# Kernel optimization log

Hardware: AMD Instinct MI355X
Metric: run time of the kernel (lower is better)

Reference implementation:

```python
import jax, jax.numpy as jnp
import numpy as np

EPS = 1e-5

def _conv1x1(x, w, b=None):
    # x: (B, Cin, H, W), w: (Cout, Cin) -> (B, Cout, H, W)
    y = jnp.einsum('bchw,oc->bohw', x, w)
    if b is not None:
        y = y + b[None, :, None, None]
    return y

def setup_inputs() -> dict:
    key = jax.random.key(0)
    ks = jax.random.split(key, 14)
    B, C, I = 4, 256, 128
    Ha = Wa = 64
    Hd = Wd = 128
    s = 0.05
    return {
        'detect':  jax.random.normal(ks[0], (B, C, Hd, Wd), jnp.float32),
        'aim':     jax.random.normal(ks[1], (B, C, Ha, Wa), jnp.float32),
        'g_w':     jax.random.normal(ks[2], (I, C), jnp.float32) * s,
        'g_b':     jax.random.normal(ks[3], (I,), jnp.float32) * s,
        'theta_w': jax.random.normal(ks[4], (I, C), jnp.float32) * s,
        'theta_b': jax.random.normal(ks[5], (I,), jnp.float32) * s,
        'phi_w':   jax.random.normal(ks[6], (I, C), jnp.float32) * s,
        'phi_b':   jax.random.normal(ks[7], (I,), jnp.float32) * s,
        'q_w':     jax.random.normal(ks[8], (C, I), jnp.float32) * s,
        'q_b':     jax.random.normal(ks[9], (C,), jnp.float32) * s,
        'bn_gamma': jax.random.normal(ks[10], (C,), jnp.float32),
        'bn_beta':  jax.random.normal(ks[11], (C,), jnp.float32),
        'bn_mean':  jax.random.normal(ks[12], (C,), jnp.float32),
        'bn_var':   jax.random.uniform(ks[13], (C,), jnp.float32) + 0.5,
    }

def reference(detect, aim, g_w, g_b, theta_w, theta_b, phi_w, phi_b,
              q_w, q_b, bn_gamma, bn_beta, bn_mean, bn_var):
    B, C, Hd, Wd = detect.shape
    _, _, Ha, Wa = aim.shape
    Na = Ha * Wa
    Nd = Hd * Wd
    I = g_w.shape[0]

    # 1x1 conv projections, flattened to token sequences
    a_g   = _conv1x1(aim, g_w, g_b).reshape(B, I, Na)        # g(aim)
    th_a  = _conv1x1(aim, theta_w, theta_b).reshape(B, I, Na)
    ph_d  = _conv1x1(detect, phi_w, phi_b).reshape(B, I, Nd)
    # (d_x = g(detect) is dead code in the original forward; omitted)

    # f = theta_x @ phi_x : (B, Na, Nd); permuted -> (B, Nd, Na); N = Na
    f = jnp.einsum('bia,bid->bad', th_a, ph_d)               # (B, Na, Nd)
    inv_n = jnp.float32(1.0 / Na)
    # non_det = (f^T / Na) @ a_x : (B, Nd, I) -> permute -> (B, I, Nd)
    non = jnp.einsum('bad,bia->bid', f * inv_n, a_g)         # (B, I, Nd)
    non = non.reshape(B, I, Hd, Wd)

    # Q: 1x1 conv (I -> C) + BatchNorm (inference mode, running stats)
    y = _conv1x1(non, q_w, q_b)
    inv_std = jax.lax.rsqrt(bn_var + EPS)
    y = (y - bn_mean[None, :, None, None]) * (bn_gamma * inv_std)[None, :, None, None] \
        + bn_beta[None, :, None, None]

    return y + detect
```

## Files before the change

### kernel.cpp

```cpp
#include <hip/hip_runtime.h>

constexpr int BB   = 4;
constexpr int CCH  = 256;
constexpr int IDIM = 128;
constexpr int NAa  = 4096;
constexpr int NDd  = 16384;
constexpr int PAD  = 320;
constexpr float NAinv = 1.0f / 4096.0f;

typedef __bf16 bf16x8 __attribute__((ext_vector_type(8)));
typedef float  f32x4  __attribute__((ext_vector_type(4)));

__device__ inline unsigned short f2bfu(float f) {
    unsigned u = __float_as_uint(f);
    u += 0x7FFFu + ((u >> 16) & 1u);
    return (unsigned short)(u >> 16);
}

__global__ __launch_bounds__(256) void k_conv(const float* __restrict__ aim,
                                              unsigned short* __restrict__ Abf,
                                              float* __restrict__ r) {
    const int row = blockIdx.x;
    const float* src = aim + (long)row * NAa;
    unsigned short* dst = Abf + (long)row * NAa;
    const int t = threadIdx.x;
    float s = 0.f;
    #pragma unroll
    for (int j = 0; j < 4; ++j) {
        const int e = (j * 256 + t) * 4;
        float4 v = *(const float4*)(src + e);
        s += v.x + v.y + v.z + v.w;
        ushort4 o; o.x = f2bfu(v.x); o.y = f2bfu(v.y); o.z = f2bfu(v.z); o.w = f2bfu(v.w);
        *(ushort4*)(dst + e) = o;
    }
    __shared__ float red[256];
    red[t] = s; __syncthreads();
    for (int st = 128; st > 0; st >>= 1) { if (t < st) red[t] += red[t + st]; __syncthreads(); }
    if (t == 0) r[row] = red[0];
}

__global__ __launch_bounds__(256) void k_prep(const float* __restrict__ qw,
                                              const float* __restrict__ gw,
                                              const float* __restrict__ gb,
                                              const float* __restrict__ thw,
                                              const float* __restrict__ thb,
                                              const float* __restrict__ phw,
                                              const float* __restrict__ phb,
                                              unsigned short* __restrict__ Ph,
                                              unsigned short* __restrict__ Rt) {
    const int idx = blockIdx.x * 256 + threadIdx.x;
    if (idx < CCH * PAD) {
        const int o = idx / PAD, c = idx - o * PAD;
        float acc = 0.f;
        if (c <= 256) {
            for (int i = 0; i < IDIM; ++i)
                acc += qw[o * IDIM + i] * ((c < 256) ? gw[i * CCH + c] : gb[i]);
        }
        Ph[idx] = f2bfu(acc);
    } else {
        const int id2 = idx - CCH * PAD;
        const int c2 = id2 / PAD, k = id2 - c2 * PAD;
        float acc = 0.f;
        if (k <= 256 && c2 <= 256) {
            for (int i = 0; i < IDIM; ++i) {
                const float av = (k < 256) ? thw[i * CCH + k] : thb[i];
                const float bv = (c2 < 256) ? phw[i * CCH + c2] : phb[i];
                acc += av * bv;
            }
        }
        Rt[id2] = f2bfu(acc);
    }
}

__global__ __launch_bounds__(64) void k_S(const unsigned short* __restrict__ Abf,
                                          float* __restrict__ Spart) {
    const int z = blockIdx.z, b = z >> 3, chunk = z & 7;
    const unsigned short* A = Abf + (long)b * CCH * NAa;
    const int lane = threadIdx.x, quad = lane >> 4, l16 = lane & 15;
    const int mb = blockIdx.y * 64, nb = blockIdx.x * 64;
    const int kb = chunk * 512;
    f32x4 acc[4][4] = {};
    for (int ks = 0; ks < 16; ++ks) {
        const int k = kb + ks * 32 + quad * 8;
        bf16x8 af[4], bfr[4];
        #pragma unroll
        for (int i = 0; i < 4; ++i) af[i]  = *(const bf16x8*)(A + (long)(mb + i * 16 + l16) * NAa + k);
        #pragma unroll
        for (int j = 0; j < 4; ++j) bfr[j] = *(const bf16x8*)(A + (long)(nb + j * 16 + l16) * NAa + k);
        #pragma unroll
        for (int i = 0; i < 4; ++i)
            #pragma unroll
            for (int j = 0; j < 4; ++j)
                acc[i][j] = __builtin_amdgcn_mfma_f32_16x16x32_bf16(af[i], bfr[j], acc[i][j], 0, 0, 0);
    }
    float* o = Spart + (long)z * CCH * CCH;
    #pragma unroll
    for (int i = 0; i < 4; ++i)
        #pragma unroll
        for (int j = 0; j < 4; ++j)
            #pragma unroll
            for (int reg = 0; reg < 4; ++reg)
                o[(long)(mb + i * 16 + quad * 4 + reg) * CCH + nb + j * 16 + l16] = acc[i][j][reg];
}

__global__ __launch_bounds__(256) void k_red(const float* __restrict__ Spart,
                                             const float* __restrict__ r,
                                             unsigned short* __restrict__ Shat) {
    const int b = blockIdx.y;
    const int idx = blockIdx.x * 256 + threadIdx.x;
    const int k = idx / PAD, n = idx - k * PAD;
    float v = 0.f;
    if (k < 256 && n < 256) {
        #pragma unroll
        for (int p = 0; p < 8; ++p)
            v += Spart[(long)(b * 8 + p) * CCH * CCH + k * CCH + n];
    } else if (k == 256 && n < 256) v = r[b * CCH + n];
    else if (n == 256 && k < 256)   v = r[b * CCH + k];
    else if (k == 256 && n == 256)  v = 4096.0f;
    Shat[(long)b * PAD * PAD + idx] = f2bfu(v);
}

__global__ __launch_bounds__(64) void k_t1(const unsigned short* __restrict__ Ph,
                                           const unsigned short* __restrict__ Sh,
                                           unsigned short* __restrict__ Th) {
    const int b = blockIdx.z;
    const unsigned short* S = Sh + (long)b * PAD * PAD;
    unsigned short* T = Th + (long)b * CCH * PAD;
    const int n0 = blockIdx.x * 64, m0 = blockIdx.y * 64;
    const int lane = threadIdx.x, quad = lane >> 4, l16 = lane & 15;
    f32x4 acc[4][4] = {};
    for (int kt = 0; kt < PAD; kt += 32) {
        bf16x8 af[4], bfr[4];
        #pragma unroll
        for (int i = 0; i < 4; ++i) af[i]  = *(const bf16x8*)(Ph + (long)(m0 + i * 16 + l16) * PAD + kt + quad * 8);
        #pragma unroll
        for (int j = 0; j < 4; ++j) bfr[j] = *(const bf16x8*)(S  + (long)(n0 + j * 16 + l16) * PAD + kt + quad * 8);
        #pragma unroll
        for (int i = 0; i < 4; ++i)
            #pragma unroll
            for (int j = 0; j < 4; ++j)
                acc[i][j] = __builtin_amdgcn_mfma_f32_16x16x32_bf16(af[i], bfr[j], acc[i][j], 0, 0, 0);
    }
    #pragma unroll
    for (int i = 0; i < 4; ++i)
        #pragma unroll
        for (int j = 0; j < 4; ++j)
            #pragma unroll
            for (int reg = 0; reg < 4; ++reg)
                T[(long)(m0 + i * 16 + quad * 4 + reg) * PAD + n0 + j * 16 + l16] = f2bfu(acc[i][j][reg]);
}

__global__ __launch_bounds__(64) void k_t2(const unsigned short* __restrict__ Th,
                                           const unsigned short* __restrict__ Rt,
                                           const float* __restrict__ qb,
                                           const float* __restrict__ gamma,
                                           const float* __restrict__ beta,
                                           const float* __restrict__ mean,
                                           const float* __restrict__ var,
                                           unsigned short* __restrict__ W5u,
                                           float* __restrict__ b5) {
    const int b = blockIdx.z;
    const unsigned short* A = Th + (long)b * CCH * PAD;
    const int n0 = blockIdx.x * 64, m0 = blockIdx.y * 64;
    const int lane = threadIdx.x, quad = lane >> 4, l16 = lane & 15;
    f32x4 acc[4][4] = {};
    for (int kt = 0; kt < PAD; kt += 32) {
        bf16x8 af[4], bfr[4];
        #pragma unroll
        for (int i = 0; i < 4; ++i) af[i]  = *(const bf16x8*)(A  + (long)(m0 + i * 16 + l16) * PAD + kt + quad * 8);
        #pragma unroll
        for (int j = 0; j < 4; ++j) bfr[j] = *(const bf16x8*)(Rt + (long)(n0 + j * 16 + l16) * PAD + kt + quad * 8);
        #pragma unroll
        for (int i = 0; i < 4; ++i)
            #pragma unroll
            for (int j = 0; j < 4; ++j)
                acc[i][j] = __builtin_amdgcn_mfma_f32_16x16x32_bf16(af[i], bfr[j], acc[i][j], 0, 0, 0);
    }
    #pragma unroll
    for (int i = 0; i < 4; ++i) {
        #pragma unroll
        for (int reg = 0; reg < 4; ++reg) {
            const int o = m0 + i * 16 + quad * 4 + reg;
            const float s = gamma[o] * rsqrtf(var[o] + 1e-5f);
            #pragma unroll
            for (int j = 0; j < 4; ++j) {
                const int c2 = n0 + j * 16 + l16;
                const float val = acc[i][j][reg] * s * NAinv;
                if (c2 < CCH)
                    W5u[((long)b * CCH + o) * CCH + c2] = f2bfu(val + (o == c2 ? 1.0f : 0.0f));
                else if (c2 == CCH)
                    b5[b * CCH + o] = val + s * (qb[o] - mean[o]) + beta[o];
            }
        }
    }
}

__global__ __launch_bounds__(256) void k_final(const float* __restrict__ D0,
                                               const unsigned short* __restrict__ W5u,
                                               const float* __restrict__ b5,
                                               float* __restrict__ out) {
    const int z = blockIdx.z;
    const int nb = blockIdx.x * 128;
    const int ob = blockIdx.y * 128;
    const float* D = D0 + (long)z * CCH * NDd;
    float* O = out + (long)z * CCH * NDd;
    const unsigned short* W = W5u + (long)z * CCH * CCH;
    const int t = threadIdx.x, wv = t >> 6, lane = t & 63, quad = lane >> 4, l16 = lane & 15;
    const int mw = (wv >> 1) * 64, nw = (wv & 1) * 64;
    const int r2 = t >> 4, g = t & 15;
    __shared__ __align__(16) unsigned short lb[2][128][40];
    f32x4 x[4];

    auto load_tile = [&](int kt) {
        const float* base = D + (long)(kt + 2 * r2) * NDd + nb + 8 * g;
        x[0] = *(const f32x4*)(base);
        x[1] = *(const f32x4*)(base + NDd);
        x[2] = *(const f32x4*)(base + 4);
        x[3] = *(const f32x4*)(base + NDd + 4);
    };
    auto write_tile = [&](int buf) {
        #pragma unroll
        for (int e2 = 0; e2 < 2; ++e2)
            #pragma unroll
            for (int c = 0; c < 4; ++c) {
                const int n = 8 * g + 4 * e2 + c;
                const int p = ((n & 7) << 4) + (n >> 3);
                const unsigned v = (unsigned)f2bfu(x[2 * e2][c]) |
                                   ((unsigned)f2bfu(x[2 * e2 + 1][c]) << 16);
                *(unsigned*)&lb[buf][p][2 * r2] = v;
            }
    };

    int pj[4];
    #pragma unroll
    for (int j = 0; j < 4; ++j) {
        const int n = nw + j * 16 + l16;
        pj[j] = ((n & 7) << 4) + (n >> 3);
    }

    f32x4 acc[4][4] = {};
    load_tile(0);
    write_tile(0);
    load_tile(32);
    for (int it = 0; it < 8; ++it) {
        __syncthreads();
        const int kt = it * 32;
        bf16x8 af[4], bfr[4];
        #pragma unroll
        for (int i = 0; i < 4; ++i)
            af[i] = *(const bf16x8*)(W + (long)(ob + mw + i * 16 + l16) * CCH + kt + quad * 8);
        #pragma unroll
        for (int j = 0; j < 4; ++j)
            bfr[j] = *(const bf16x8*)&lb[it & 1][pj[j]][quad * 8];
        #pragma unroll
        for (int i = 0; i < 4; ++i)
            #pragma unroll
            for (int j = 0; j < 4; ++j)
                acc[i][j] = __builtin_amdgcn_mfma_f32_16x16x32_bf16(af[i], bfr[j], acc[i][j], 0, 0, 0);
        if (it < 7) {
            write_tile((it + 1) & 1);
            if (it < 6) load_tile((it + 2) * 32);
        }
    }
    #pragma unroll
    for (int i = 0; i < 4; ++i) {
        float bv[4];
        #pragma unroll
        for (int reg = 0; reg < 4; ++reg)
            bv[reg] = b5[z * CCH + ob + mw + i * 16 + quad * 4 + reg];
        #pragma unroll
        for (int j = 0; j < 4; ++j) {
            const int n = nb + nw + j * 16 + l16;
            #pragma unroll
            for (int reg = 0; reg < 4; ++reg)
                O[(long)(ob + mw + i * 16 + quad * 4 + reg) * NDd + n] = acc[i][j][reg] + bv[reg];
        }
    }
}

extern "C" void kernel_launch(void* const* d_in, const int* in_sizes, int n_in,
                              void* d_out, int out_size, void* d_ws, size_t ws_size,
                              hipStream_t stream) {
    const float* detect = (const float*)d_in[0];
    const float* aim    = (const float*)d_in[1];
    const float* g_w    = (const float*)d_in[2];
    const float* g_b    = (const float*)d_in[3];
    const float* th_w   = (const float*)d_in[4];
    const float* th_b   = (const float*)d_in[5];
    const float* phi_w  = (const float*)d_in[6];
    const float* phi_b  = (const float*)d_in[7];
    const float* q_w    = (const float*)d_in[8];
    const float* q_b    = (const float*)d_in[9];
    const float* gamma  = (const float*)d_in[10];
    const float* beta   = (const float*)d_in[11];
    const float* mean   = (const float*)d_in[12];
    const float* var    = (const float*)d_in[13];
    float* out = (float*)d_out;

    float* ws = (float*)d_ws;
    unsigned short* Abf = (unsigned short*)ws;
    float* r     = ws + 2097152;
    float* Spart = r + 1024;
    unsigned short* ub = (unsigned short*)(Spart + 2097152);
    unsigned short* Shat_u  = ub;
    unsigned short* Phat_u  = Shat_u + 409600;
    unsigned short* RhatT_u = Phat_u + 81920;
    unsigned short* That_u  = RhatT_u + 102400;
    unsigned short* W5u     = That_u + 327680;
    float* b5 = (float*)(W5u + 262144);

    k_prep<<<dim3((CCH * PAD + PAD * PAD) / 256), dim3(256), 0, stream>>>(
        q_w, g_w, g_b, th_w, th_b, phi_w, phi_b, Phat_u, RhatT_u);
    k_conv<<<dim3(BB * CCH), dim3(256), 0, stream>>>(aim, Abf, r);
    k_S<<<dim3(4, 4, BB * 8), dim3(64), 0, stream>>>(Abf, Spart);
    k_red<<<dim3(PAD * PAD / 256, BB), dim3(256), 0, stream>>>(Spart, r, Shat_u);
    k_t1<<<dim3(5, 4, BB), dim3(64), 0, stream>>>(Phat_u, Shat_u, That_u);
    k_t2<<<dim3(5, 4, BB), dim3(64), 0, stream>>>(That_u, RhatT_u, q_b, gamma, beta, mean, var, W5u, b5);
    k_final<<<dim3(NDd / 128, CCH / 128, BB), dim3(256), 0, stream>>>(detect, W5u, b5, out);
}
```

Measured before the change: 218.3 us.

## Merge front kernels, fuse T1/T2 via LDS, split S finer, simplify final load

Merges the aim conversion and weight-prep kernels into one launch, and fuses the two small 320-wide GEMMs (k_t1/k_t2) into a single kernel that keeps the intermediate T tile in shared memory instead of global. It also doubles the K-split of the Gram-matrix kernel to 16 chunks for more parallelism, at the cost of a larger partial-sum buffer and reduction. The final kernel drops its double-buffered LDS staging of detect and instead loads strided fp32 values directly into registers and packs them to bf16. The direct loads are column-strided per lane and may lose coalescing compared with the previous staged path.

```diff
diff --git a/kernel.cpp b/kernel.cpp
--- a/kernel.cpp
+++ b/kernel.cpp
@@ -17,70 +17,71 @@
     return (unsigned short)(u >> 16);
 }
 
-__global__ __launch_bounds__(256) void k_conv(const float* __restrict__ aim,
-                                              unsigned short* __restrict__ Abf,
-                                              float* __restrict__ r) {
-    const int row = blockIdx.x;
-    const float* src = aim + (long)row * NAa;
-    unsigned short* dst = Abf + (long)row * NAa;
+__global__ __launch_bounds__(256) void k_front(const float* __restrict__ aim,
+                                               unsigned short* __restrict__ Abf,
+                                               float* __restrict__ r,
+                                               const float* __restrict__ qw,
+                                               const float* __restrict__ gw,
+                                               const float* __restrict__ gb,
+                                               const float* __restrict__ thw,
+                                               const float* __restrict__ thb,
+                                               const float* __restrict__ phw,
+                                               const float* __restrict__ phb,
+                                               unsigned short* __restrict__ Ph,
+                                               unsigned short* __restrict__ Rt) {
     const int t = threadIdx.x;
-    float s = 0.f;
-    #pragma unroll
-    for (int j = 0; j < 4; ++j) {
-        const int e = (j * 256 + t) * 4;
-        float4 v = *(const float4*)(src + e);
-        s += v.x + v.y + v.z + v.w;
-        ushort4 o; o.x = f2bfu(v.x); o.y = f2bfu(v.y); o.z = f2bfu(v.z); o.w = f2bfu(v.w);
-        *(ushort4*)(dst + e) = o;
-    }
-    __shared__ float red[256];
-    red[t] = s; __syncthreads();
-    for (int st = 128; st > 0; st >>= 1) { if (t < st) red[t] += red[t + st]; __syncthreads(); }
-    if (t == 0) r[row] = red[0];
-}
-
-__global__ __launch_bounds__(256) void k_prep(const float* __restrict__ qw,
-                                              const float* __restrict__ gw,
-                                              const float* __restrict__ gb,
-                                              const float* __restrict__ thw,
-                                              const float* __restrict__ thb,
-                                              const float* __restrict__ phw,
-                                              const float* __restrict__ phb,
-                                              unsigned short* __restrict__ Ph,
-                                              unsigned short* __restrict__ Rt) {
-    const int idx = blockIdx.x * 256 + threadIdx.x;
-    if (idx < CCH * PAD) {
-        const int o = idx / PAD, c = idx - o * PAD;
-        float acc = 0.f;
-        if (c <= 256) {
-            for (int i = 0; i < IDIM; ++i)
-                acc += qw[o * IDIM + i] * ((c < 256) ? gw[i * CCH + c] : gb[i]);
-        }
-        Ph[idx] = f2bfu(acc);
+    if (blockIdx.x < BB * CCH) {
+        const int row = blockIdx.x;
+        const float* src = aim + (long)row * NAa;
+        unsigned short* dst = Abf + (long)row * NAa;
+        float s = 0.f;
+        #pragma unroll
+        for (int j = 0; j < 4; ++j) {
+            const int e = (j * 256 + t) * 4;
+            float4 v = *(const float4*)(src + e);
+            s += v.x + v.y + v.z + v.w;
+            ushort4 o; o.x = f2bfu(v.x); o.y = f2bfu(v.y); o.z = f2bfu(v.z); o.w = f2bfu(v.w);
+            *(ushort4*)(dst + e) = o;
+        }
+        __shared__ float red[256];
+        red[t] = s; __syncthreads();
+        for (int st = 128; st > 0; st >>= 1) { if (t < st) red[t] += red[t + st]; __syncthreads(); }
+        if (t == 0) r[row] = red[0];
     } else {
-        const int id2 = idx - CCH * PAD;
-        const int c2 = id2 / PAD, k = id2 - c2 * PAD;
-        float acc = 0.f;
-        if (k <= 256 && c2 <= 256) {
-            for (int i = 0; i < IDIM; ++i) {
-                const float av = (k < 256) ? thw[i * CCH + k] : thb[i];
-                const float bv = (c2 < 256) ? phw[i * CCH + c2] : phb[i];
-                acc += av * bv;
+        const int idx = (blockIdx.x - BB * CCH) * 256 + t;
+        if (idx < CCH * PAD) {
+            const int o = idx / PAD, c = idx - o * PAD;
+            float acc = 0.f;
+            if (c <= 256) {
+                for (int i = 0; i < IDIM; ++i)
+                    acc += qw[o * IDIM + i] * ((c < 256) ? gw[i * CCH + c] : gb[i]);
             }
-        }
-        Rt[id2] = f2bfu(acc);
+            Ph[idx] = f2bfu(acc);
+        } else {
+            const int id2 = idx - CCH * PAD;
+            const int c2 = id2 / PAD, k = id2 - c2 * PAD;
+            float acc = 0.f;
+            if (k <= 256 && c2 <= 256) {
+                for (int i = 0; i < IDIM; ++i) {
+                    const float av = (k < 256) ? thw[i * CCH + k] : thb[i];
+                    const float bv = (c2 < 256) ? phw[i * CCH + c2] : phb[i];
+                    acc += av * bv;
+                }
+            }
+            Rt[id2] = f2bfu(acc);
+        }
     }
 }
 
 __global__ __launch_bounds__(64) void k_S(const unsigned short* __restrict__ Abf,
                                           float* __restrict__ Spart) {
-    const int z = blockIdx.z, b = z >> 3, chunk = z & 7;
+    const int z = blockIdx.z, b = z >> 4, chunk = z & 15;
     const unsigned short* A = Abf + (long)b * CCH * NAa;
     const int lane = threadIdx.x, quad = lane >> 4, l16 = lane & 15;
     const int mb = blockIdx.y * 64, nb = blockIdx.x * 64;
-    const int kb = chunk * 512;
+    const int kb = chunk * 256;
     f32x4 acc[4][4] = {};
-    for (int ks = 0; ks < 16; ++ks) {
+    for (int ks = 0; ks < 8; ++ks) {
         const int k = kb + ks * 32 + quad * 8;
         bf16x8 af[4], bfr[4];
         #pragma unroll
@@ -112,86 +113,86 @@
     float v = 0.f;
     if (k < 256 && n < 256) {
         #pragma unroll
-        for (int p = 0; p < 8; ++p)
-            v += Spart[(long)(b * 8 + p) * CCH * CCH + k * CCH + n];
+        for (int p = 0; p < 16; ++p)
+            v += Spart[(long)(b * 16 + p) * CCH * CCH + k * CCH + n];
     } else if (k == 256 && n < 256) v = r[b * CCH + n];
     else if (n == 256 && k < 256)   v = r[b * CCH + k];
     else if (k == 256 && n == 256)  v = 4096.0f;
     Shat[(long)b * PAD * PAD + idx] = f2bfu(v);
 }
 
-__global__ __launch_bounds__(64) void k_t1(const unsigned short* __restrict__ Ph,
-                                           const unsigned short* __restrict__ Sh,
-                                           unsigned short* __restrict__ Th) {
-    const int b = blockIdx.z;
+__global__ __launch_bounds__(256) void k_w5f(const unsigned short* __restrict__ Ph,
+                                             const unsigned short* __restrict__ Sh,
+                                             const unsigned short* __restrict__ Rt,
+                                             const float* __restrict__ qb,
+                                             const float* __restrict__ gamma,
+                                             const float* __restrict__ beta,
+                                             const float* __restrict__ mean,
+                                             const float* __restrict__ var,
+                                             unsigned short* __restrict__ W5u,
+                                             float* __restrict__ b5) {
+    const int b = blockIdx.y, m0 = blockIdx.x * 64;
     const unsigned short* S = Sh + (long)b * PAD * PAD;
-    unsigned short* T = Th + (long)b * CCH * PAD;
-    const int n0 = blockIdx.x * 64, m0 = blockIdx.y * 64;
-    const int lane = threadIdx.x, quad = lane >> 4, l16 = lane & 15;
-    f32x4 acc[4][4] = {};
-    for (int kt = 0; kt < PAD; kt += 32) {
-        bf16x8 af[4], bfr[4];
-        #pragma unroll
-        for (int i = 0; i < 4; ++i) af[i]  = *(const bf16x8*)(Ph + (long)(m0 + i * 16 + l16) * PAD + kt + quad * 8);
-        #pragma unroll
-        for (int j = 0; j < 4; ++j) bfr[j] = *(const bf16x8*)(S  + (long)(n0 + j * 16 + l16) * PAD + kt + quad * 8);
-        #pragma unroll
-        for (int i = 0; i < 4; ++i)
-            #pragma unroll
-            for (int j = 0; j < 4; ++j)
-                acc[i][j] = __builtin_amdgcn_mfma_f32_16x16x32_bf16(af[i], bfr[j], acc[i][j], 0, 0, 0);
-    }
-    #pragma unroll
-    for (int i = 0; i < 4; ++i)
-        #pragma unroll
-        for (int j = 0; j < 4; ++j)
-            #pragma unroll
-            for (int reg = 0; reg < 4; ++reg)
-                T[(long)(m0 + i * 16 + quad * 4 + reg) * PAD + n0 + j * 16 + l16] = f2bfu(acc[i][j][reg]);
-}
-
-__global__ __launch_bounds__(64) void k_t2(const unsigned short* __restrict__ Th,
-                                           const unsigned short* __restrict__ Rt,
-                                           const float* __restrict__ qb,
-                                           const float* __restrict__ gamma,
-                                           const float* __restrict__ beta,
-                                           const float* __restrict__ mean,
-                                           const float* __restrict__ var,
-                                           unsigned short* __restrict__ W5u,
-                                           float* __restrict__ b5) {
-    const int b = blockIdx.z;
-    const unsigned short* A = Th + (long)b * CCH * PAD;
-    const int n0 = blockIdx.x * 64, m0 = blockIdx.y * 64;
-    const int lane = threadIdx.x, quad = lane >> 4, l16 = lane & 15;
-    f32x4 acc[4][4] = {};
-    for (int kt = 0; kt < PAD; kt += 32) {
-        bf16x8 af[4], bfr[4];
-        #pragma unroll
-        for (int i = 0; i < 4; ++i) af[i]  = *(const bf16x8*)(A  + (long)(m0 + i * 16 + l16) * PAD + kt + quad * 8);
-        #pragma unroll
-        for (int j = 0; j < 4; ++j) bfr[j] = *(const bf16x8*)(Rt + (long)(n0 + j * 16 + l16) * PAD + kt + quad * 8);
-        #pragma unroll
-        for (int i = 0; i < 4; ++i)
-            #pragma unroll
-            for (int j = 0; j < 4; ++j)
-                acc[i][j] = __builtin_amdgcn_mfma_f32_16x16x32_bf16(af[i], bfr[j], acc[i][j], 0, 0, 0);
-    }
-    #pragma unroll
-    for (int i = 0; i < 4; ++i) {
-        #pragma unroll
-        for (int reg = 0; reg < 4; ++reg) {
-            const int o = m0 + i * 16 + quad * 4 + reg;
-            const float s = gamma[o] * rsqrtf(var[o] + 1e-5f);
-            #pragma unroll
-            for (int j = 0; j < 4; ++j) {
-                const int c2 = n0 + j * 16 + l16;
-                const float val = acc[i][j][reg] * s * NAinv;
-                if (c2 < CCH)
-                    W5u[((long)b * CCH + o) * CCH + c2] = f2bfu(val + (o == c2 ? 1.0f : 0.0f));
-                else if (c2 == CCH)
-                    b5[b * CCH + o] = val + s * (qb[o] - mean[o]) + beta[o];
+    const int t = threadIdx.x, w = t >> 6, lane = t & 63, quad = lane >> 4, l16 = lane & 15;
+    __shared__ __align__(16) unsigned short Tl[64][PAD];
+
+    for (int nt = w; nt < 5; nt += 4) {
+        f32x4 acc[4][4] = {};
+        for (int kt = 0; kt < PAD; kt += 32) {
+            bf16x8 af[4], bfr[4];
+            #pragma unroll
+            for (int i = 0; i < 4; ++i)
+                af[i]  = *(const bf16x8*)(Ph + (long)(m0 + i * 16 + l16) * PAD + kt + quad * 8);
+            #pragma unroll
+            for (int j = 0; j < 4; ++j)
+                bfr[j] = *(const bf16x8*)(S + (long)(nt * 64 + j * 16 + l16) * PAD + kt + quad * 8);
+            #pragma unroll
+            for (int i = 0; i < 4; ++i)
+                #pragma unroll
+                for (int j = 0; j < 4; ++j)
+                    acc[i][j] = __builtin_amdgcn_mfma_f32_16x16x32_bf16(af[i], bfr[j], acc[i][j], 0, 0, 0);
+        }
+        #pragma unroll
+        for (int i = 0; i < 4; ++i)
+            #pragma unroll
+            for (int j = 0; j < 4; ++j)
+                #pragma unroll
+                for (int reg = 0; reg < 4; ++reg)
+                    Tl[i * 16 + quad * 4 + reg][nt * 64 + j * 16 + l16] = f2bfu(acc[i][j][reg]);
+    }
+    __syncthreads();
+    for (int nt = w; nt < 5; nt += 4) {
+        f32x4 acc[4][4] = {};
+        for (int kt = 0; kt < PAD; kt += 32) {
+            bf16x8 af[4], bfr[4];
+            #pragma unroll
+            for (int i = 0; i < 4; ++i)
+                af[i]  = *(const bf16x8*)(&Tl[i * 16 + l16][kt + quad * 8]);
+            #pragma unroll
+            for (int j = 0; j < 4; ++j)
+                bfr[j] = *(const bf16x8*)(Rt + (long)(nt * 64 + j * 16 + l16) * PAD + kt + quad * 8);
+            #pragma unroll
+            for (int i = 0; i < 4; ++i)
+                #pragma unroll
+                for (int j = 0; j < 4; ++j)
+                    acc[i][j] = __builtin_amdgcn_mfma_f32_16x16x32_bf16(af[i], bfr[j], acc[i][j], 0, 0, 0);
+        }
+        #pragma unroll
+        for (int i = 0; i < 4; ++i)
+            #pragma unroll
+            for (int reg = 0; reg < 4; ++reg) {
+                const int o = m0 + i * 16 + quad * 4 + reg;
+                const float s = gamma[o] * rsqrtf(var[o] + 1e-5f);
+                #pragma unroll
+                for (int j = 0; j < 4; ++j) {
+                    const int c2 = nt * 64 + j * 16 + l16;
+                    const float val = acc[i][j][reg] * s * NAinv;
+                    if (c2 < CCH)
+                        W5u[((long)b * CCH + o) * CCH + c2] = f2bfu(val + (o == c2 ? 1.0f : 0.0f));
+                    else if (c2 == CCH)
+                        b5[b * CCH + o] = val + s * (qb[o] - mean[o]) + beta[o];
+                }
             }
-        }
     }
 }
 
@@ -207,60 +208,34 @@
     const unsigned short* W = W5u + (long)z * CCH * CCH;
     const int t = threadIdx.x, wv = t >> 6, lane = t & 63, quad = lane >> 4, l16 = lane & 15;
     const int mw = (wv >> 1) * 64, nw = (wv & 1) * 64;
-    const int r2 = t >> 4, g = t & 15;
-    __shared__ __align__(16) unsigned short lb[2][128][40];
-    f32x4 x[4];
-
-    auto load_tile = [&](int kt) {
-        const float* base = D + (long)(kt + 2 * r2) * NDd + nb + 8 * g;
-        x[0] = *(const f32x4*)(base);
-        x[1] = *(const f32x4*)(base + NDd);
-        x[2] = *(const f32x4*)(base + 4);
-        x[3] = *(const f32x4*)(base + NDd + 4);
-    };
-    auto write_tile = [&](int buf) {
-        #pragma unroll
-        for (int e2 = 0; e2 < 2; ++e2)
-            #pragma unroll
-            for (int c = 0; c < 4; ++c) {
-                const int n = 8 * g + 4 * e2 + c;
-                const int p = ((n & 7) << 4) + (n >> 3);
-                const unsigned v = (unsigned)f2bfu(x[2 * e2][c]) |
-                                   ((unsigned)f2bfu(x[2 * e2 + 1][c]) << 16);
-                *(unsigned*)&lb[buf][p][2 * r2] = v;
-            }
-    };
-
-    int pj[4];
+    int nj[4];
     #pragma unroll
-    for (int j = 0; j < 4; ++j) {
-        const int n = nw + j * 16 + l16;
-        pj[j] = ((n & 7) << 4) + (n >> 3);
-    }
+    for (int j = 0; j < 4; ++j) nj[j] = nb + nw + j * 16 + l16;
 
     f32x4 acc[4][4] = {};
-    load_tile(0);
-    write_tile(0);
-    load_tile(32);
-    for (int it = 0; it < 8; ++it) {
-        __syncthreads();
-        const int kt = it * 32;
-        bf16x8 af[4], bfr[4];
+    for (int kt = 0; kt < CCH; kt += 32) {
+        const float* Dk = D + (long)(kt + quad * 8) * NDd;
+        bf16x8 bfr[4];
+        #pragma unroll
+        for (int j = 0; j < 4; ++j) {
+            float xv[8];
+            #pragma unroll
+            for (int e = 0; e < 8; ++e) xv[e] = Dk[(long)e * NDd + nj[j]];
+            union { unsigned u[4]; bf16x8 v; } pk;
+            #pragma unroll
+            for (int pp = 0; pp < 4; ++pp)
+                pk.u[pp] = (unsigned)f2bfu(xv[2 * pp]) | ((unsigned)f2bfu(xv[2 * pp + 1]) << 16);
+            bfr[j] = pk.v;
+        }
+        bf16x8 af[4];
         #pragma unroll
         for (int i = 0; i < 4; ++i)
             af[i] = *(const bf16x8*)(W + (long)(ob + mw + i * 16 + l16) * CCH + kt + quad * 8);
         #pragma unroll
-        for (int j = 0; j < 4; ++j)
-            bfr[j] = *(const bf16x8*)&lb[it & 1][pj[j]][quad * 8];
-        #pragma unroll
         for (int i = 0; i < 4; ++i)
             #pragma unroll
             for (int j = 0; j < 4; ++j)
                 acc[i][j] = __builtin_amdgcn_mfma_f32_16x16x32_bf16(af[i], bfr[j], acc[i][j], 0, 0, 0);
-        if (it < 7) {
-            write_tile((it + 1) & 1);
-            if (it < 6) load_tile((it + 2) * 32);
-        }
     }
     #pragma unroll
     for (int i = 0; i < 4; ++i) {
@@ -301,20 +276,19 @@
     unsigned short* Abf = (unsigned short*)ws;
     float* r     = ws + 2097152;
     float* Spart = r + 1024;
-    unsigned short* ub = (unsigned short*)(Spart + 2097152);
+    unsigned short* ub = (unsigned short*)(Spart + 4194304);
     unsigned short* Shat_u  = ub;
     unsigned short* Phat_u  = Shat_u + 409600;
     unsigned short* RhatT_u = Phat_u + 81920;
-    unsigned short* That_u  = RhatT_u + 102400;
-    unsigned short* W5u     = That_u + 327680;
+    unsigned short* W5u     = RhatT_u + 102400;
     float* b5 = (float*)(W5u + 262144);
 
-    k_prep<<<dim3((CCH * PAD + PAD * PAD) / 256), dim3(256), 0, stream>>>(
-        q_w, g_w, g_b, th_w, th_b, phi_w, phi_b, Phat_u, RhatT_u);
-    k_conv<<<dim3(BB * CCH), dim3(256), 0, stream>>>(aim, Abf, r);
-    k_S<<<dim3(4, 4, BB * 8), dim3(64), 0, stream>>>(Abf, Spart);
+    const int prep_blocks = (CCH * PAD + PAD * PAD) / 256;
+    k_front<<<dim3(BB * CCH + prep_blocks), dim3(256), 0, stream>>>(
+        aim, Abf, r, q_w, g_w, g_b, th_w, th_b, phi_w, phi_b, Phat_u, RhatT_u);
+    k_S<<<dim3(4, 4, BB * 16), dim3(64), 0, stream>>>(Abf, Spart);
     k_red<<<dim3(PAD * PAD / 256, BB), dim3(256), 0, stream>>>(Spart, r, Shat_u);
-    k_t1<<<dim3(5, 4, BB), dim3(64), 0, stream>>>(Phat_u, Shat_u, That_u);
-    k_t2<<<dim3(5, 4, BB), dim3(64), 0, stream>>>(That_u, RhatT_u, q_b, gamma, beta, mean, var, W5u, b5);
+    k_w5f<<<dim3(4, BB), dim3(256), 0, stream>>>(
+        Phat_u, Shat_u, RhatT_u, q_b, gamma, beta, mean, var, W5u, b5);
     k_final<<<dim3(NDd / 128, CCH / 128, BB), dim3(256), 0, stream>>>(detect, W5u, b5, out);
 }
```

Result: slower. 248.3 us (+13.8%).
